# Performance work log

Measured on AMD Instinct MI355X. Metric: run time of the kernel, lower is better.

Reference implementation:

```python
import jax, jax.numpy as jnp
import numpy as np

V = 32000   # vocab
D = 512     # embed dim
H = 512     # hidden dim
K = 5       # beam size
SOS, EOS, PAD = 0, 1, 2
NEG = -1e30  # acts as -inf but keeps grads NaN-free


def gru_cell(x, h, Wih, Whh, bih, bhh):
    # torch nn.GRU cell convention: gates ordered (r, z, n)
    gi = x @ Wih.T + bih
    gh = h @ Whh.T + bhh
    i_r, i_z, i_n = jnp.split(gi, 3, axis=-1)
    h_r, h_z, h_n = jnp.split(gh, 3, axis=-1)
    r = jax.nn.sigmoid(i_r + h_r)
    z = jax.nn.sigmoid(i_z + h_z)
    n = jnp.tanh(i_n + r * h_n)
    return (1.0 - z) * n + z * h


def setup_inputs() -> dict:
    key = jax.random.key(0)
    ks = jax.random.split(key, 14)
    s = 0.02
    f = jnp.float32
    return {
        "source": jax.random.randint(ks[0], (32, 32), 0, V, dtype=jnp.int32),
        "emb_src": jax.random.normal(ks[1], (V, D), f) * s,
        "emb_tgt": jax.random.normal(ks[2], (V, D), f) * s,
        "enc_Wih": jax.random.normal(ks[3], (3 * H, D), f) * s,
        "enc_Whh": jax.random.normal(ks[4], (3 * H, H), f) * s,
        "enc_bih": jnp.zeros((3 * H,), f),
        "enc_bhh": jnp.zeros((3 * H,), f),
        "dec_Wih": jax.random.normal(ks[5], (3 * H, D), f) * s,
        "dec_Whh": jax.random.normal(ks[6], (3 * H, H), f) * s,
        "dec_bih": jnp.zeros((3 * H,), f),
        "dec_bhh": jnp.zeros((3 * H,), f),
        "W_out": jax.random.normal(ks[7], (H, V), f) * s,
        "b_out": jnp.zeros((V,), f),
    }


def beam_search(source, emb_src, emb_tgt, enc_Wih, enc_Whh, enc_bih, enc_bhh,
                dec_Wih, dec_Whh, dec_bih, dec_bhh, W_out, b_out):
    B, S = source.shape
    T = S + 1  # max decode steps (while counter < source.shape[1] + 1)

    # ---- encoder: 1-layer GRU over source tokens ----
    xs = jnp.swapaxes(emb_src[source], 0, 1)  # [S, B, D]
    def enc_step(h, x):
        return gru_cell(x, h, enc_Wih, enc_Whh, enc_bih, enc_bhh), None
    h_enc, _ = jax.lax.scan(enc_step, jnp.zeros((B, H), xs.dtype), xs)
    # initialize_h: repeat each sentence's hidden state beam_size times
    hidden = jnp.broadcast_to(h_enc[:, None, :], (B, K, H))  # [B, K, H]

    def dec_logprobs(tok, hid):
        x = emb_tgt[tok]  # [B, K, D]
        h1 = gru_cell(x, hid, dec_Wih, dec_Whh, dec_bih, dec_bhh)
        lp = jax.nn.log_softmax(h1 @ W_out + b_out, axis=-1)  # [B, K, V]
        return lp, h1

    # ---- step 0: initial_advance (top-K words from one SOS row) ----
    lp, h1 = dec_logprobs(jnp.zeros((B, K), jnp.int32), hidden)
    vals, words = jax.lax.top_k(lp[:, 0, :], K)  # [B, K]
    seqs = jnp.full((B, K, T + 1), PAD, jnp.int32)
    seqs = seqs.at[:, :, 0].set(SOS).at[:, :, 1].set(words)
    act_ll = vals
    hidden = h1  # all beams identical at step 0
    best_ll = jnp.full((B,), NEG, vals.dtype)
    best_seq = jnp.full((B, T + 1), PAD, jnp.int32)
    pos = jnp.arange(T + 1)
    bidx = jnp.arange(B)

    # ---- steps 1..T-1: advance. Dead beam slots carry NEG likelihood,
    # which reproduces the shrinking-active-set math of the original. ----
    def step(carry, t):
        seqs, act_ll, hidden, last_tok, best_ll, best_seq = carry
        lp, h1 = dec_logprobs(last_tok, hidden)
        L = (act_ll[:, :, None] + lp).reshape(B, K * V)
        vals, idx = jax.lax.top_k(L, K)
        parent = idx // V           # seq_ind
        word = idx % V              # word_ind
        gathered = jnp.take_along_axis(seqs, parent[:, :, None], axis=1)
        new_seqs = jnp.where(pos[None, None, :] == t + 1, word[:, :, None], gathered)
        finite = vals > NEG * 0.5
        is_eos = (word == EOS) & finite
        # completed likelihood normalized by candidate length (t+2 tokens)
        comp_ll = jnp.where(is_eos, vals / (t.astype(vals.dtype) + 2.0), NEG)
        cbest = comp_ll.max(axis=1)
        cseq = new_seqs[bidx, comp_ll.argmax(axis=1)]  # [B, T+1], PAD-padded
        improve = cbest > best_ll
        best_ll = jnp.where(improve, cbest, best_ll)
        best_seq = jnp.where(improve[:, None], cseq, best_seq)
        act_ll = jnp.where(finite & ~is_eos, vals, NEG)
        hidden = jnp.take_along_axis(h1, parent[:, :, None], axis=1)  # arrange_h gather
        return (new_seqs, act_ll, hidden, word, best_ll, best_seq), None

    carry = (seqs, act_ll, hidden, words, best_ll, best_seq)
    carry, _ = jax.lax.scan(step, carry, jnp.arange(1, T))
    seqs, act_ll, hidden, last_tok, best_ll, best_seq = carry

    # return_winner: best completed if any, else best active
    have = best_ll > NEG * 0.5
    act_best = act_ll.argmax(axis=1)
    act_seq = seqs[bidx, act_best]
    winner = jnp.where(have[:, None], best_seq, act_seq)  # [B, T+1]
    winner_ll = jnp.where(have, best_ll, act_ll.max(axis=1))
    return winner, winner_ll


def reference(source, emb_src, emb_tgt, enc_Wih, enc_Whh, enc_bih, enc_bhh,
              dec_Wih, dec_Whh, dec_bih, dec_bhh, W_out, b_out):
    winner, _ = beam_search(source, emb_src, emb_tgt, enc_Wih, enc_Whh, enc_bih,
                            enc_bhh, dec_Wih, dec_Whh, dec_bih, dec_bhh, W_out, b_out)
    return winner
```

## Files before the change

kernel.cpp:

```cpp
#include <hip/hip_runtime.h>
#include <math.h>

#define NEGF   (-1e30f)
#define FINTH  (-5e29f)
#define VSZ    32000
#define KBM    5
#define SEQL   34
#define NVBLK  1000

__device__ __forceinline__ bool cand_gt(float av, int ai, float bv, int bi) {
  return (av > bv) || (av == bv && ai < bi);
}

#define INS5(xx, ii)                                                           \
  if (cand_gt(xx, ii, tv4, ti4)) {                                             \
    tv4 = xx; ti4 = ii;                                                        \
    if (cand_gt(tv4, ti4, tv3, ti3)) { float tf = tv3; int tj = ti3; tv3 = tv4; ti3 = ti4; tv4 = tf; ti4 = tj; \
      if (cand_gt(tv3, ti3, tv2, ti2)) { tf = tv2; tj = ti2; tv2 = tv3; ti2 = ti3; tv3 = tf; ti3 = tj; \
        if (cand_gt(tv2, ti2, tv1, ti1)) { tf = tv1; tj = ti1; tv1 = tv2; ti1 = ti2; tv2 = tf; ti2 = tj; \
          if (cand_gt(tv1, ti1, tv0, ti0)) { tf = tv0; tj = ti0; tv0 = tv1; ti0 = ti1; tv1 = tf; ti1 = tj; } } } } }

struct T5 { float v[5]; int i[5]; };

__device__ __forceinline__ void t5_init(T5& t) {
  #pragma unroll
  for (int j = 0; j < 5; j++) { t.v[j] = -3.4e38f; t.i[j] = 0x7fffffff; }
}

__device__ __forceinline__ void t5_ins(T5& t, float x, int id) {
  if (cand_gt(x, id, t.v[4], t.i[4])) {
    t.v[4] = x; t.i[4] = id;
    #pragma unroll
    for (int j = 4; j > 0; j--) {
      if (cand_gt(t.v[j], t.i[j], t.v[j-1], t.i[j-1])) {
        float tf = t.v[j-1]; int tj = t.i[j-1];
        t.v[j-1] = t.v[j]; t.i[j-1] = t.i[j];
        t.v[j] = tf; t.i[j] = tj;
      }
    }
  }
}

__device__ __forceinline__ T5 t5_merge(const T5& a, const T5& b) {
  T5 r;
  int i = 0, j = 0;
  #pragma unroll
  for (int o = 0; o < 5; o++) {
    float avv = a.v[i]; int aii = a.i[i];
    float bvv = b.v[j]; int bii = b.i[j];
    bool ta = cand_gt(avv, aii, bvv, bii);
    r.v[o] = ta ? avv : bvv; r.i[o] = ta ? aii : bii;
    i += ta ? 1 : 0; j += ta ? 0 : 1;
  }
  return r;
}

__global__ void init_kernel(float* hb0, int* word_buf, int* hsrc) {
  int i = blockIdx.x * 256 + threadIdx.x;
  if (i < 32 * 512) hb0[i] = 0.f;
  if (i < 160) { word_buf[i] = 0; hsrc[i] = i / KBM; }
}

__global__ __launch_bounds__(256, 4) void genc_kernel(
    const float* __restrict__ emb, const int* __restrict__ source,
    const float* __restrict__ Wih, float* __restrict__ gi_enc)
{
  const int tid = threadIdx.x;
  const int ng = tid & 7;
  const int mg = tid >> 3;
  const int j0 = blockIdx.x * 16 + ng * 2;
  const int r0 = blockIdx.y * 128 + mg * 4;

  const float* arow[4];
  #pragma unroll
  for (int i = 0; i < 4; i++) {
    int r = r0 + i;
    int tok = source[(r & 31) * 32 + (r >> 5)];
    arow[i] = emb + (long)tok * 512;
  }
  const float* w0p = Wih + (long)j0 * 512;
  const float* w1p = w0p + 512;

  float acc0[4], acc1[4];
  #pragma unroll
  for (int i = 0; i < 4; i++) { acc0[i] = 0.f; acc1[i] = 0.f; }

  float4 wc0 = *(const float4*)w0p;
  float4 wc1 = *(const float4*)w1p;
  float4 ac[4];
  #pragma unroll
  for (int i = 0; i < 4; i++) ac[i] = *(const float4*)arow[i];

  for (int k = 0; k < 508; k += 4) {
    float4 wn0 = *(const float4*)(w0p + k + 4);
    float4 wn1 = *(const float4*)(w1p + k + 4);
    float4 an[4];
    #pragma unroll
    for (int i = 0; i < 4; i++) an[i] = *(const float4*)(arow[i] + k + 4);
    #pragma unroll
    for (int i = 0; i < 4; i++) {
      acc0[i] += ac[i].x * wc0.x + ac[i].y * wc0.y + ac[i].z * wc0.z + ac[i].w * wc0.w;
      acc1[i] += ac[i].x * wc1.x + ac[i].y * wc1.y + ac[i].z * wc1.z + ac[i].w * wc1.w;
    }
    wc0 = wn0; wc1 = wn1;
    #pragma unroll
    for (int i = 0; i < 4; i++) ac[i] = an[i];
  }
  #pragma unroll
  for (int i = 0; i < 4; i++) {
    acc0[i] += ac[i].x * wc0.x + ac[i].y * wc0.y + ac[i].z * wc0.z + ac[i].w * wc0.w;
    acc1[i] += ac[i].x * wc1.x + ac[i].y * wc1.y + ac[i].z * wc1.z + ac[i].w * wc1.w;
  }
  #pragma unroll
  for (int i = 0; i < 4; i++) {
    float2 r; r.x = acc0[i]; r.y = acc1[i];
    *(float2*)(gi_enc + (long)(r0 + i) * 1536 + j0) = r;
  }
}

template<int P, int HONLY>
__global__ __launch_bounds__(256, 4) void gates_kernel(
    const float* __restrict__ emb, const int* __restrict__ tok_ptr, int tok_stride,
    const float* __restrict__ hbuf, const int* __restrict__ hsrc,
    const float* __restrict__ Wih, const float* __restrict__ Whh,
    float* __restrict__ gip, float* __restrict__ ghp)
{
  const bool is_h = HONLY ? true : (blockIdx.y != 0);
  const float* W = is_h ? Whh : Wih;
  const int M = 32 * P;
  float* out = (is_h ? ghp : gip) + (long)blockIdx.z * M * 1536;

  const int tid = threadIdx.x;
  const int ng = tid & 7;
  const int mg = tid >> 3;
  const int j0 = blockIdx.x * 16 + ng * 2;
  const int k0 = blockIdx.z * 128;

  const float* arow[P];
  #pragma unroll
  for (int i = 0; i < P; i++) {
    int m = mg * P + i;
    if (is_h) { int r = hsrc ? hsrc[m] : m; arow[i] = hbuf + (long)r * 512 + k0; }
    else      { int tk = tok_ptr[m * tok_stride]; arow[i] = emb + (long)tk * 512 + k0; }
  }
  const float* w0p = W + (long)j0 * 512 + k0;
  const float* w1p = w0p + 512;

  float acc0[P], acc1[P];
  #pragma unroll
  for (int i = 0; i < P; i++) { acc0[i] = 0.f; acc1[i] = 0.f; }

  float4 wc0 = *(const float4*)w0p;
  float4 wc1 = *(const float4*)w1p;
  float4 ac[P];
  #pragma unroll
  for (int i = 0; i < P; i++) ac[i] = *(const float4*)arow[i];

  for (int k = 0; k < 124; k += 4) {
    float4 wn0 = *(const float4*)(w0p + k + 4);
    float4 wn1 = *(const float4*)(w1p + k + 4);
    float4 an[P];
    #pragma unroll
    for (int i = 0; i < P; i++) an[i] = *(const float4*)(arow[i] + k + 4);
    #pragma unroll
    for (int i = 0; i < P; i++) {
      acc0[i] += ac[i].x * wc0.x + ac[i].y * wc0.y + ac[i].z * wc0.z + ac[i].w * wc0.w;
      acc1[i] += ac[i].x * wc1.x + ac[i].y * wc1.y + ac[i].z * wc1.z + ac[i].w * wc1.w;
    }
    wc0 = wn0; wc1 = wn1;
    #pragma unroll
    for (int i = 0; i < P; i++) ac[i] = an[i];
  }
  #pragma unroll
  for (int i = 0; i < P; i++) {
    acc0[i] += ac[i].x * wc0.x + ac[i].y * wc0.y + ac[i].z * wc0.z + ac[i].w * wc0.w;
    acc1[i] += ac[i].x * wc1.x + ac[i].y * wc1.y + ac[i].z * wc1.z + ac[i].w * wc1.w;
  }
  #pragma unroll
  for (int i = 0; i < P; i++) {
    int m = mg * P + i;
    float2 r; r.x = acc0[i]; r.y = acc1[i];
    *(float2*)(out + (long)m * 1536 + j0) = r;
  }
}

template<int NPI, int NPH, int M>
__global__ __launch_bounds__(256) void hupd_kernel(
    const float* __restrict__ gip, const float* __restrict__ ghp,
    const float* __restrict__ bih, const float* __restrict__ bhh,
    const float* __restrict__ hin, const int* __restrict__ hsrc,
    float* __restrict__ hout)
{
  int idx = blockIdx.x * 256 + threadIdx.x;
  if (idx >= M * 512) return;
  int m = idx >> 9, i = idx & 511;
  float ir = 0.f, iz = 0.f, inn = 0.f, hr = 0.f, hz = 0.f, hn = 0.f;
  #pragma unroll
  for (int p = 0; p < NPI; p++) {
    const float* g = gip + (long)p * M * 1536 + (long)m * 1536;
    ir += g[i]; iz += g[512 + i]; inn += g[1024 + i];
  }
  #pragma unroll
  for (int p = 0; p < NPH; p++) {
    const float* g = ghp + (long)p * M * 1536 + (long)m * 1536;
    hr += g[i]; hz += g[512 + i]; hn += g[1024 + i];
  }
  ir += bih[i]; iz += bih[512 + i]; inn += bih[1024 + i];
  hr += bhh[i]; hz += bhh[512 + i]; hn += bhh[1024 + i];
  float r = 1.f / (1.f + expf(-(ir + hr)));
  float z = 1.f / (1.f + expf(-(iz + hz)));
  float n = tanhf(inn + r * hn);
  int src = hsrc ? hsrc[m] : m;
  float h = hin[(long)src * 512 + i];
  hout[(long)m * 512 + i] = (1.f - z) * n + z * h;
}

__global__ __launch_bounds__(256, 4) void logtop_kernel(
    const float* __restrict__ h1, const float* __restrict__ Wout,
    const float* __restrict__ bout, float* __restrict__ PK)
{
  const int tid = threadIdx.x;
  const int ng = tid & 7;
  const int mg = tid >> 3;
  const int blk = blockIdx.x;
  const int v0 = blk * 32;
  const int v = v0 + ng * 4;
  const int m0 = mg * 5;

  __shared__ float Wlds[2][2048];
  __shared__ float L[160][33];

  const float* a0 = h1 + (long)m0 * 512;

  const int skk = tid >> 3;
  const int sv4 = tid & 7;
  const float* sg0 = Wout + (size_t)skk * VSZ + v0 + sv4 * 4;
  const float* sg1 = Wout + (size_t)(32 + skk) * VSZ + v0 + sv4 * 4;
  const int lwave = (tid >> 6) * 256;

  auto stage = [&](int tt, int bb) {
    const float* g0 = sg0 + (size_t)tt * 64 * VSZ;
    const float* g1 = sg1 + (size_t)tt * 64 * VSZ;
    __builtin_amdgcn_global_load_lds(
        (const __attribute__((address_space(1))) void*)g0,
        (__attribute__((address_space(3))) void*)&Wlds[bb][lwave], 16, 0, 0);
    __builtin_amdgcn_global_load_lds(
        (const __attribute__((address_space(1))) void*)g1,
        (__attribute__((address_space(3))) void*)&Wlds[bb][1024 + lwave], 16, 0, 0);
  };

  float4 acc[5];
  #pragma unroll
  for (int i = 0; i < 5; i++) acc[i] = make_float4(0.f, 0.f, 0.f, 0.f);

  stage(0, 0);
  __syncthreads();

  float4 aA[5], aB[5];
  #pragma unroll
  for (int i = 0; i < 5; i++) aA[i] = *(const float4*)(a0 + i * 512);

  for (int t8 = 0; t8 < 8; t8++) {
    const float* lb = &Wlds[t8 & 1][0];
    if (t8 < 7) stage(t8 + 1, (t8 + 1) & 1);
    const int kt = t8 * 64;
    #pragma unroll 1
    for (int c = 0; c < 16; c += 2) {
      const int k = kt + c * 4;
      float4 w0[4], w1[4];
      #pragma unroll
      for (int j = 0; j < 4; j++) w0[j] = *(const float4*)&lb[(c * 4 + j) * 32 + ng * 4];
      #pragma unroll
      for (int j = 0; j < 4; j++) w1[j] = *(const float4*)&lb[(c * 4 + 4 + j) * 32 + ng * 4];
      #pragma unroll
      for (int i = 0; i < 5; i++) aB[i] = *(const float4*)(a0 + i * 512 + k + 4);
      #pragma unroll
      for (int i = 0; i < 5; i++) {
        acc[i].x += aA[i].x * w0[0].x + aA[i].y * w0[1].x + aA[i].z * w0[2].x + aA[i].w * w0[3].x;
        acc[i].y += aA[i].x * w0[0].y + aA[i].y * w0[1].y + aA[i].z * w0[2].y + aA[i].w * w0[3].y;
        acc[i].z += aA[i].x * w0[0].z + aA[i].y * w0[1].z + aA[i].z * w0[2].z + aA[i].w * w0[3].z;
        acc[i].w += aA[i].x * w0[0].w + aA[i].y * w0[1].w + aA[i].z * w0[2].w + aA[i].w * w0[3].w;
      }
      int kn = k + 8; if (kn >= 512) kn = 0;
      #pragma unroll
      for (int i = 0; i < 5; i++) aA[i] = *(const float4*)(a0 + i * 512 + kn);
      #pragma unroll
      for (int i = 0; i < 5; i++) {
        acc[i].x += aB[i].x * w1[0].x + aB[i].y * w1[1].x + aB[i].z * w1[2].x + aB[i].w * w1[3].x;
        acc[i].y += aB[i].x * w1[0].y + aB[i].y * w1[1].y + aB[i].z * w1[2].y + aB[i].w * w1[3].y;
        acc[i].z += aB[i].x * w1[0].z + aB[i].y * w1[1].z + aB[i].z * w1[2].z + aB[i].w * w1[3].z;
        acc[i].w += aB[i].x * w1[0].w + aB[i].y * w1[1].w + aB[i].z * w1[2].w + aB[i].w * w1[3].w;
      }
    }
    __syncthreads();
  }

  float4 bb4 = *(const float4*)(bout + v);
  #pragma unroll
  for (int i = 0; i < 5; i++) {
    L[m0 + i][ng * 4 + 0] = acc[i].x + bb4.x;
    L[m0 + i][ng * 4 + 1] = acc[i].y + bb4.y;
    L[m0 + i][ng * 4 + 2] = acc[i].z + bb4.z;
    L[m0 + i][ng * 4 + 3] = acc[i].w + bb4.w;
  }
  __syncthreads();

  if (tid < 160) {
    float m = -3.4e38f, s = 0.f;
    float tv0 = -3.4e38f, tv1 = -3.4e38f, tv2 = -3.4e38f, tv3 = -3.4e38f, tv4 = -3.4e38f;
    int ti0 = 0x7fffffff, ti1 = 0x7fffffff, ti2 = 0x7fffffff, ti3 = 0x7fffffff, ti4 = 0x7fffffff;
    int base = blk * 32;
    for (int c = 0; c < 32; c++) {
      float x = L[tid][c];
      if (x > m) { s *= expf(m - x); m = x; }
      s += expf(x - m);
      INS5(x, base + c);
    }
    float* pk = PK + ((long)blk * 160 + tid) * 16;
    float4 q0 = make_float4(m, s, tv0, tv1);
    float4 q1 = make_float4(tv2, tv3, tv4, __int_as_float(ti0));
    float4 q2 = make_float4(__int_as_float(ti1), __int_as_float(ti2),
                            __int_as_float(ti3), __int_as_float(ti4));
    *(float4*)(pk + 0) = q0;
    *(float4*)(pk + 4) = q1;
    *(float4*)(pk + 8) = q2;
  }
}

__global__ __launch_bounds__(256) void rowmerge_kernel(
    const float* __restrict__ PK, float* __restrict__ RW)
{
  const int row = blockIdx.x, tid = threadIdx.x;
  float m = -3.4e38f, s = 0.f;
  T5 t; t5_init(t);

  for (int it = 0; it < 4; it++) {
    int blk = tid + it * 256;
    if (blk >= NVBLK) break;
    const float* pk = PK + ((long)blk * 160 + row) * 16;
    float4 q0 = *(const float4*)(pk + 0);
    float4 q1 = *(const float4*)(pk + 4);
    float4 q2 = *(const float4*)(pk + 8);
    float nm = fmaxf(m, q0.x);
    s = s * expf(m - nm) + q0.y * expf(q0.x - nm);
    m = nm;
    t5_ins(t, q0.z, __float_as_int(q1.w));
    t5_ins(t, q0.w, __float_as_int(q2.x));
    t5_ins(t, q1.x, __float_as_int(q2.y));
    t5_ins(t, q1.y, __float_as_int(q2.z));
    t5_ins(t, q1.z, __float_as_int(q2.w));
  }

  for (int mask = 1; mask < 64; mask <<= 1) {
    float om = __shfl_xor(m, mask, 64);
    float os = __shfl_xor(s, mask, 64);
    float nm = fmaxf(m, om);
    s = s * expf(m - nm) + os * expf(om - nm);
    m = nm;
    T5 o;
    #pragma unroll
    for (int j = 0; j < 5; j++) {
      o.v[j] = __shfl_xor(t.v[j], mask, 64);
      o.i[j] = __shfl_xor(t.i[j], mask, 64);
    }
    t = t5_merge(t, o);
  }

  __shared__ float wm[4], wss[4], wv[4][5];
  __shared__ int   wi[4][5];
  const int wave = tid >> 6;
  if ((tid & 63) == 0) {
    wm[wave] = m; wss[wave] = s;
    #pragma unroll
    for (int j = 0; j < 5; j++) { wv[wave][j] = t.v[j]; wi[wave][j] = t.i[j]; }
  }
  __syncthreads();
  if (tid == 0) {
    float M2 = wm[0], S2 = wss[0];
    #pragma unroll
    for (int w = 1; w < 4; w++) {
      float nm = fmaxf(M2, wm[w]);
      S2 = S2 * expf(M2 - nm) + wss[w] * expf(wm[w] - nm);
      M2 = nm;
    }
    T5 r;
    #pragma unroll
    for (int j = 0; j < 5; j++) { r.v[j] = wv[0][j]; r.i[j] = wi[0][j]; }
    #pragma unroll
    for (int w = 1; w < 4; w++) {
      T5 o;
      #pragma unroll
      for (int j = 0; j < 5; j++) { o.v[j] = wv[w][j]; o.i[j] = wi[w][j]; }
      r = t5_merge(r, o);
    }
    float* rw = RW + (long)row * 16;
    rw[0] = M2 + logf(S2);
    #pragma unroll
    for (int j = 0; j < 5; j++) {
      rw[1 + j] = r.v[j];
      rw[6 + j] = __int_as_float(r.i[j]);
    }
  }
}

__global__ void book0_kernel(const float* __restrict__ RW,
                             int* __restrict__ seqs, float* __restrict__ act_ll,
                             int* __restrict__ word_buf, int* __restrict__ hsrc,
                             float* __restrict__ best_ll, int* __restrict__ best_seq)
{
  int b = blockIdx.x, tid = threadIdx.x;
  const float* rw = RW + (long)(b * KBM) * 16;
  float l = rw[0];
  if (tid < SEQL) {
    for (int j = 0; j < KBM; j++) {
      int w = __float_as_int(rw[6 + j]);
      seqs[(b * KBM + j) * SEQL + tid] = (tid == 0) ? 0 : (tid == 1 ? w : 2);
    }
    best_seq[b * SEQL + tid] = 2;
  }
  if (tid < KBM) {
    act_ll[b * KBM + tid] = rw[1 + tid] - l;
    word_buf[b * KBM + tid] = __float_as_int(rw[6 + tid]);
    hsrc[b * KBM + tid] = b * KBM + tid;
  }
  if (tid == 0) best_ll[b] = NEGF;
}

__global__ void book_kernel(const float* __restrict__ RW,
                            const int* __restrict__ seqs_old, int* __restrict__ seqs_new,
                            float* __restrict__ act_ll, int* __restrict__ word_buf,
                            int* __restrict__ hsrc, float* __restrict__ best_ll,
                            int* __restrict__ best_seq, int t)
{
  int b = blockIdx.x, tid = threadIdx.x;
  __shared__ float sv5[5];
  __shared__ int   si5[5];
  if (tid == 0) {
    T5 g; t5_init(g);
    #pragma unroll
    for (int k = 0; k < KBM; k++) {
      const float* rw = RW + (long)(b * KBM + k) * 16;
      float a = act_ll[b * KBM + k], l = rw[0];
      #pragma unroll
      for (int j = 0; j < 5; j++) {
        float x = a + (rw[1 + j] - l);
        int id = k * VSZ + __float_as_int(rw[6 + j]);
        t5_ins(g, x, id);
      }
    }
    #pragma unroll
    for (int j = 0; j < 5; j++) { sv5[j] = g.v[j]; si5[j] = g.i[j]; }
  }
  __syncthreads();

  __shared__ int ls[KBM][SEQL];
  float v[KBM]; int pr[KBM], wd[KBM];
  #pragma unroll
  for (int j = 0; j < KBM; j++) {
    v[j] = sv5[j];
    int id = si5[j];
    pr[j] = id / VSZ; wd[j] = id % VSZ;
  }
  #pragma unroll
  for (int j = 0; j < KBM; j++) {
    if (tid < SEQL) {
      int x = (tid == t + 1) ? wd[j] : seqs_old[(b * KBM + pr[j]) * SEQL + tid];
      ls[j][tid] = x;
      seqs_new[(b * KBM + j) * SEQL + tid] = x;
    }
  }
  __syncthreads();
  float cll[KBM];
  #pragma unroll
  for (int j = 0; j < KBM; j++) {
    bool fin = v[j] > FINTH;
    bool eos = (wd[j] == 1) && fin;
    cll[j] = eos ? v[j] / (float)(t + 2) : NEGF;
  }
  int jb = 0; float cb = cll[0];
  #pragma unroll
  for (int j = 1; j < KBM; j++) if (cll[j] > cb) { cb = cll[j]; jb = j; }
  bool improve = cb > best_ll[b];
  if (improve) {
    if (tid == 0) best_ll[b] = cb;
    if (tid < SEQL) best_seq[b * SEQL + tid] = ls[jb][tid];
  }
  if (tid < KBM) {
    int j = tid;
    bool fin = v[j] > FINTH;
    bool eos = (wd[j] == 1) && fin;
    act_ll[b * KBM + j] = (fin && !eos) ? v[j] : NEGF;
    word_buf[b * KBM + j] = wd[j];
    hsrc[b * KBM + j] = b * KBM + pr[j];
  }
}

__global__ void final_kernel(const float* __restrict__ best_ll, const int* __restrict__ best_seq,
                             const float* __restrict__ act_ll, const int* __restrict__ seqs,
                             int* __restrict__ out)
{
  int b = blockIdx.x, tid = threadIdx.x;
  bool have = best_ll[b] > FINTH;
  int jb = 0; float ab = act_ll[b * KBM];
  for (int j = 1; j < KBM; j++)
    if (act_ll[b * KBM + j] > ab) { ab = act_ll[b * KBM + j]; jb = j; }
  if (tid < SEQL)
    out[b * SEQL + tid] = have ? best_seq[b * SEQL + tid]
                               : seqs[(b * KBM + jb) * SEQL + tid];
}

extern "C" void kernel_launch(void* const* d_in, const int* in_sizes, int n_in,
                              void* d_out, int out_size, void* d_ws, size_t ws_size,
                              hipStream_t stream)
{
  const int*   source  = (const int*)d_in[0];
  const float* emb_src = (const float*)d_in[1];
  const float* emb_tgt = (const float*)d_in[2];
  const float* eWih = (const float*)d_in[3];
  const float* eWhh = (const float*)d_in[4];
  const float* ebih = (const float*)d_in[5];
  const float* ebhh = (const float*)d_in[6];
  const float* dWih = (const float*)d_in[7];
  const float* dWhh = (const float*)d_in[8];
  const float* dbih = (const float*)d_in[9];
  const float* dbhh = (const float*)d_in[10];
  const float* Wout = (const float*)d_in[11];
  const float* bout = (const float*)d_in[12];
  int* out = (int*)d_out;

  char* ws = (char*)d_ws;
  size_t off = 0;
  auto alloc = [&](size_t bytes) {
    void* p = ws + off;
    off = (off + bytes + 255) & ~(size_t)255;
    return p;
  };
  float* hb0     = (float*)alloc(160 * 512 * 4);
  float* hb1     = (float*)alloc(160 * 512 * 4);
  float* gip     = (float*)alloc((size_t)4 * 160 * 1536 * 4);
  float* ghp     = (float*)alloc((size_t)4 * 160 * 1536 * 4);
  char*  uni     = (char*) alloc((size_t)11 * 1024 * 1024);
  float* gi_enc  = (float*)uni;
  float* PK      = (float*)uni;
  float* RW      = (float*)alloc(160 * 16 * 4);
  float* act_ll  = (float*)alloc(160 * 4);
  float* best_ll = (float*)alloc(32 * 4);
  int*   seqs0   = (int*)alloc(160 * SEQL * 4);
  int*   seqs1   = (int*)alloc(160 * SEQL * 4);
  int*   wordb   = (int*)alloc(160 * 4);
  int*   hsrc    = (int*)alloc(160 * 4);
  int*   bseq    = (int*)alloc(32 * SEQL * 4);

  init_kernel<<<64, 256, 0, stream>>>(hb0, wordb, hsrc);

  genc_kernel<<<dim3(96, 8), 256, 0, stream>>>(emb_src, source, eWih, gi_enc);
  for (int s = 0; s < 32; s++) {
    gates_kernel<1, 1><<<dim3(96, 1, 4), 256, 0, stream>>>(
        nullptr, nullptr, 0, hb0, nullptr, nullptr, eWhh, nullptr, ghp);
    hupd_kernel<1, 4, 32><<<64, 256, 0, stream>>>(
        gi_enc + (size_t)s * 32 * 1536, ghp, ebih, ebhh, hb0, nullptr, hb0);
  }

  gates_kernel<5, 0><<<dim3(96, 2, 4), 256, 0, stream>>>(
      emb_tgt, wordb, 1, hb0, hsrc, dWih, dWhh, gip, ghp);
  hupd_kernel<4, 4, 160><<<320, 256, 0, stream>>>(
      gip, ghp, dbih, dbhh, hb0, hsrc, hb1);
  logtop_kernel<<<NVBLK, 256, 0, stream>>>(hb1, Wout, bout, PK);
  rowmerge_kernel<<<160, 256, 0, stream>>>(PK, RW);
  book0_kernel<<<32, 64, 0, stream>>>(RW, seqs0, act_ll, wordb, hsrc,
                                      best_ll, bseq);

  float* hcur = hb1; float* hoth = hb0;
  int* scur = seqs0; int* soth = seqs1;
  for (int t = 1; t <= 32; t++) {
    gates_kernel<5, 0><<<dim3(96, 2, 4), 256, 0, stream>>>(
        emb_tgt, wordb, 1, hcur, hsrc, dWih, dWhh, gip, ghp);
    hupd_kernel<4, 4, 160><<<320, 256, 0, stream>>>(
        gip, ghp, dbih, dbhh, hcur, hsrc, hoth);
    logtop_kernel<<<NVBLK, 256, 0, stream>>>(hoth, Wout, bout, PK);
    rowmerge_kernel<<<160, 256, 0, stream>>>(PK, RW);
    book_kernel<<<32, 64, 0, stream>>>(RW, scur, soth, act_ll, wordb,
                                       hsrc, best_ll, bseq, t);
    { float* tmp = hcur; hcur = hoth; hoth = tmp; }
    { int* tmp = scur; scur = soth; soth = tmp; }
  }

  final_kernel<<<32, 64, 0, stream>>>(best_ll, bseq, act_ll, scur, out);
}
```

Measured before the change: 7.120 ms.

## Halve logtop block size with ten rows per thread, split-K encoder GEMM, transpose PK layout

The vocab projection kernel now runs 128 threads per block, each computing 10 beam rows instead of 5. This doubles register reuse of each LDS weight load, and the staging loop issues four async global-to-LDS loads per thread. The encoder input GEMM is split along K into two halves written to separate partial buffers, which the encoder hidden update sums, giving twice as many blocks. The per-block top-k partials are stored row-major (row, block) so rowmerge reads them contiguously. The trade-off is higher register pressure in logtop and an extra partial buffer read per encoder step.

```diff
diff --git a/kernel.cpp b/kernel.cpp
--- a/kernel.cpp
+++ b/kernel.cpp
@@ -70,15 +70,17 @@
   const int mg = tid >> 3;
   const int j0 = blockIdx.x * 16 + ng * 2;
   const int r0 = blockIdx.y * 128 + mg * 4;
+  const int k0 = blockIdx.z * 256;
+  float* out = gi_enc + (long)blockIdx.z * 1024 * 1536;
 
   const float* arow[4];
   #pragma unroll
   for (int i = 0; i < 4; i++) {
     int r = r0 + i;
     int tok = source[(r & 31) * 32 + (r >> 5)];
-    arow[i] = emb + (long)tok * 512;
-  }
-  const float* w0p = Wih + (long)j0 * 512;
+    arow[i] = emb + (long)tok * 512 + k0;
+  }
+  const float* w0p = Wih + (long)j0 * 512 + k0;
   const float* w1p = w0p + 512;
 
   float acc0[4], acc1[4];
@@ -91,7 +93,7 @@
   #pragma unroll
   for (int i = 0; i < 4; i++) ac[i] = *(const float4*)arow[i];
 
-  for (int k = 0; k < 508; k += 4) {
+  for (int k = 0; k < 252; k += 4) {
     float4 wn0 = *(const float4*)(w0p + k + 4);
     float4 wn1 = *(const float4*)(w1p + k + 4);
     float4 an[4];
@@ -114,7 +116,7 @@
   #pragma unroll
   for (int i = 0; i < 4; i++) {
     float2 r; r.x = acc0[i]; r.y = acc1[i];
-    *(float2*)(gi_enc + (long)(r0 + i) * 1536 + j0) = r;
+    *(float2*)(out + (long)(r0 + i) * 1536 + j0) = r;
   }
 }
 
@@ -189,7 +191,7 @@
     const float* __restrict__ gip, const float* __restrict__ ghp,
     const float* __restrict__ bih, const float* __restrict__ bhh,
     const float* __restrict__ hin, const int* __restrict__ hsrc,
-    float* __restrict__ hout)
+    float* __restrict__ hout, long gist)
 {
   int idx = blockIdx.x * 256 + threadIdx.x;
   if (idx >= M * 512) return;
@@ -197,7 +199,7 @@
   float ir = 0.f, iz = 0.f, inn = 0.f, hr = 0.f, hz = 0.f, hn = 0.f;
   #pragma unroll
   for (int p = 0; p < NPI; p++) {
-    const float* g = gip + (long)p * M * 1536 + (long)m * 1536;
+    const float* g = gip + (long)p * gist + (long)m * 1536;
     ir += g[i]; iz += g[512 + i]; inn += g[1024 + i];
   }
   #pragma unroll
@@ -215,7 +217,7 @@
   hout[(long)m * 512 + i] = (1.f - z) * n + z * h;
 }
 
-__global__ __launch_bounds__(256, 4) void logtop_kernel(
+__global__ __launch_bounds__(128, 4) void logtop_kernel(
     const float* __restrict__ h1, const float* __restrict__ Wout,
     const float* __restrict__ bout, float* __restrict__ PK)
 {
@@ -225,40 +227,38 @@
   const int blk = blockIdx.x;
   const int v0 = blk * 32;
   const int v = v0 + ng * 4;
-  const int m0 = mg * 5;
+  const int m0 = mg * 10;
 
   __shared__ float Wlds[2][2048];
   __shared__ float L[160][33];
 
   const float* a0 = h1 + (long)m0 * 512;
 
-  const int skk = tid >> 3;
-  const int sv4 = tid & 7;
-  const float* sg0 = Wout + (size_t)skk * VSZ + v0 + sv4 * 4;
-  const float* sg1 = Wout + (size_t)(32 + skk) * VSZ + v0 + sv4 * 4;
-  const int lwave = (tid >> 6) * 256;
+  const int l = tid & 63;
+  const int wv = tid >> 6;
+  const int kkb = wv * 8 + (l >> 3);
+  const int sv4 = l & 7;
 
   auto stage = [&](int tt, int bb) {
-    const float* g0 = sg0 + (size_t)tt * 64 * VSZ;
-    const float* g1 = sg1 + (size_t)tt * 64 * VSZ;
-    __builtin_amdgcn_global_load_lds(
-        (const __attribute__((address_space(1))) void*)g0,
-        (__attribute__((address_space(3))) void*)&Wlds[bb][lwave], 16, 0, 0);
-    __builtin_amdgcn_global_load_lds(
-        (const __attribute__((address_space(1))) void*)g1,
-        (__attribute__((address_space(3))) void*)&Wlds[bb][1024 + lwave], 16, 0, 0);
+    #pragma unroll
+    for (int p = 0; p < 4; p++) {
+      const float* g = Wout + (size_t)(tt * 64 + p * 16 + kkb) * VSZ + v0 + sv4 * 4;
+      __builtin_amdgcn_global_load_lds(
+          (const __attribute__((address_space(1))) void*)g,
+          (__attribute__((address_space(3))) void*)&Wlds[bb][p * 512 + wv * 256], 16, 0, 0);
+    }
   };
 
-  float4 acc[5];
-  #pragma unroll
-  for (int i = 0; i < 5; i++) acc[i] = make_float4(0.f, 0.f, 0.f, 0.f);
+  float4 acc[10];
+  #pragma unroll
+  for (int i = 0; i < 10; i++) acc[i] = make_float4(0.f, 0.f, 0.f, 0.f);
 
   stage(0, 0);
   __syncthreads();
 
-  float4 aA[5], aB[5];
-  #pragma unroll
-  for (int i = 0; i < 5; i++) aA[i] = *(const float4*)(a0 + i * 512);
+  float4 aA[10], aB[10];
+  #pragma unroll
+  for (int i = 0; i < 10; i++) aA[i] = *(const float4*)(a0 + i * 512);
 
   for (int t8 = 0; t8 < 8; t8++) {
     const float* lb = &Wlds[t8 & 1][0];
@@ -273,9 +273,9 @@
       #pragma unroll
       for (int j = 0; j < 4; j++) w1[j] = *(const float4*)&lb[(c * 4 + 4 + j) * 32 + ng * 4];
       #pragma unroll
-      for (int i = 0; i < 5; i++) aB[i] = *(const float4*)(a0 + i * 512 + k + 4);
-      #pragma unroll
-      for (int i = 0; i < 5; i++) {
+      for (int i = 0; i < 10; i++) aB[i] = *(const float4*)(a0 + i * 512 + k + 4);
+      #pragma unroll
+      for (int i = 0; i < 10; i++) {
         acc[i].x += aA[i].x * w0[0].x + aA[i].y * w0[1].x + aA[i].z * w0[2].x + aA[i].w * w0[3].x;
         acc[i].y += aA[i].x * w0[0].y + aA[i].y * w0[1].y + aA[i].z * w0[2].y + aA[i].w * w0[3].y;
         acc[i].z += aA[i].x * w0[0].z + aA[i].y * w0[1].z + aA[i].z * w0[2].z + aA[i].w * w0[3].z;
@@ -283,9 +283,9 @@
       }
       int kn = k + 8; if (kn >= 512) kn = 0;
       #pragma unroll
-      for (int i = 0; i < 5; i++) aA[i] = *(const float4*)(a0 + i * 512 + kn);
-      #pragma unroll
-      for (int i = 0; i < 5; i++) {
+      for (int i = 0; i < 10; i++) aA[i] = *(const float4*)(a0 + i * 512 + kn);
+      #pragma unroll
+      for (int i = 0; i < 10; i++) {
         acc[i].x += aB[i].x * w1[0].x + aB[i].y * w1[1].x + aB[i].z * w1[2].x + aB[i].w * w1[3].x;
         acc[i].y += aB[i].x * w1[0].y + aB[i].y * w1[1].y + aB[i].z * w1[2].y + aB[i].w * w1[3].y;
         acc[i].z += aB[i].x * w1[0].z + aB[i].y * w1[1].z + aB[i].z * w1[2].z + aB[i].w * w1[3].z;
@@ -297,7 +297,7 @@
 
   float4 bb4 = *(const float4*)(bout + v);
   #pragma unroll
-  for (int i = 0; i < 5; i++) {
+  for (int i = 0; i < 10; i++) {
     L[m0 + i][ng * 4 + 0] = acc[i].x + bb4.x;
     L[m0 + i][ng * 4 + 1] = acc[i].y + bb4.y;
     L[m0 + i][ng * 4 + 2] = acc[i].z + bb4.z;
@@ -305,18 +305,18 @@
   }
   __syncthreads();
 
-  if (tid < 160) {
+  for (int r = tid; r < 160; r += 128) {
     float m = -3.4e38f, s = 0.f;
     float tv0 = -3.4e38f, tv1 = -3.4e38f, tv2 = -3.4e38f, tv3 = -3.4e38f, tv4 = -3.4e38f;
     int ti0 = 0x7fffffff, ti1 = 0x7fffffff, ti2 = 0x7fffffff, ti3 = 0x7fffffff, ti4 = 0x7fffffff;
     int base = blk * 32;
     for (int c = 0; c < 32; c++) {
-      float x = L[tid][c];
+      float x = L[r][c];
       if (x > m) { s *= expf(m - x); m = x; }
       s += expf(x - m);
       INS5(x, base + c);
     }
-    float* pk = PK + ((long)blk * 160 + tid) * 16;
+    float* pk = PK + ((long)r * NVBLK + blk) * 16;
     float4 q0 = make_float4(m, s, tv0, tv1);
     float4 q1 = make_float4(tv2, tv3, tv4, __int_as_float(ti0));
     float4 q2 = make_float4(__int_as_float(ti1), __int_as_float(ti2),
@@ -337,7 +337,7 @@
   for (int it = 0; it < 4; it++) {
     int blk = tid + it * 256;
     if (blk >= NVBLK) break;
-    const float* pk = PK + ((long)blk * 160 + row) * 16;
+    const float* pk = PK + ((long)row * NVBLK + blk) * 16;
     float4 q0 = *(const float4*)(pk + 0);
     float4 q1 = *(const float4*)(pk + 4);
     float4 q2 = *(const float4*)(pk + 8);
@@ -539,7 +539,7 @@
   float* hb1     = (float*)alloc(160 * 512 * 4);
   float* gip     = (float*)alloc((size_t)4 * 160 * 1536 * 4);
   float* ghp     = (float*)alloc((size_t)4 * 160 * 1536 * 4);
-  char*  uni     = (char*) alloc((size_t)11 * 1024 * 1024);
+  char*  uni     = (char*) alloc((size_t)13 * 1024 * 1024);
   float* gi_enc  = (float*)uni;
   float* PK      = (float*)uni;
   float* RW      = (float*)alloc(160 * 16 * 4);
@@ -553,19 +553,20 @@
 
   init_kernel<<<64, 256, 0, stream>>>(hb0, wordb, hsrc);
 
-  genc_kernel<<<dim3(96, 8), 256, 0, stream>>>(emb_src, source, eWih, gi_enc);
+  genc_kernel<<<dim3(96, 8, 2), 256, 0, stream>>>(emb_src, source, eWih, gi_enc);
   for (int s = 0; s < 32; s++) {
     gates_kernel<1, 1><<<dim3(96, 1, 4), 256, 0, stream>>>(
         nullptr, nullptr, 0, hb0, nullptr, nullptr, eWhh, nullptr, ghp);
-    hupd_kernel<1, 4, 32><<<64, 256, 0, stream>>>(
-        gi_enc + (size_t)s * 32 * 1536, ghp, ebih, ebhh, hb0, nullptr, hb0);
+    hupd_kernel<2, 4, 32><<<64, 256, 0, stream>>>(
+        gi_enc + (size_t)s * 32 * 1536, ghp, ebih, ebhh, hb0, nullptr, hb0,
+        (long)1024 * 1536);
   }
 
   gates_kernel<5, 0><<<dim3(96, 2, 4), 256, 0, stream>>>(
       emb_tgt, wordb, 1, hb0, hsrc, dWih, dWhh, gip, ghp);
   hupd_kernel<4, 4, 160><<<320, 256, 0, stream>>>(
-      gip, ghp, dbih, dbhh, hb0, hsrc, hb1);
-  logtop_kernel<<<NVBLK, 256, 0, stream>>>(hb1, Wout, bout, PK);
+      gip, ghp, dbih, dbhh, hb0, hsrc, hb1, (long)160 * 1536);
+  logtop_kernel<<<NVBLK, 128, 0, stream>>>(hb1, Wout, bout, PK);
   rowmerge_kernel<<<160, 256, 0, stream>>>(PK, RW);
   book0_kernel<<<32, 64, 0, stream>>>(RW, seqs0, act_ll, wordb, hsrc,
                                       best_ll, bseq);
@@ -576,8 +577,8 @@
     gates_kernel<5, 0><<<dim3(96, 2, 4), 256, 0, stream>>>(
         emb_tgt, wordb, 1, hcur, hsrc, dWih, dWhh, gip, ghp);
     hupd_kernel<4, 4, 160><<<320, 256, 0, stream>>>(
-        gip, ghp, dbih, dbhh, hcur, hsrc, hoth);
-    logtop_kernel<<<NVBLK, 256, 0, stream>>>(hoth, Wout, bout, PK);
+        gip, ghp, dbih, dbhh, hcur, hsrc, hoth, (long)160 * 1536);
+    logtop_kernel<<<NVBLK, 128, 0, stream>>>(hoth, Wout, bout, PK);
     rowmerge_kernel<<<160, 256, 0, stream>>>(PK, RW);
     book_kernel<<<32, 64, 0, stream>>>(RW, scur, soth, act_ll, wordb,
                                        hsrc, best_ll, bseq, t);
```

New measurement: 7.619 ms. 7.0% more time.
